# Kernel optimization log

Measured on AMD Instinct MI355X. Metric: run time of the kernel, lower is better.

Reference implementation:

```python
import jax, jax.numpy as jnp
import numpy as np

FRACTION = 0.33  # from attn_type='query_selector_0.33'


def setup_inputs() -> dict:
    key = jax.random.key(0)
    k1, k2, k3, k4 = jax.random.split(key, 4)
    B, L, DIM_VAL, DIM_ATTN = 8, 4096, 64, 64
    scale = 1.0 / np.sqrt(DIM_VAL).astype(np.float32)
    x = jax.random.normal(k1, (B, L, DIM_VAL), dtype=jnp.float32)
    Wq = jax.random.normal(k2, (DIM_VAL, DIM_ATTN), dtype=jnp.float32) * scale
    Wk = jax.random.normal(k3, (DIM_VAL, DIM_ATTN), dtype=jnp.float32) * scale
    Wv = jax.random.normal(k4, (DIM_VAL, DIM_VAL), dtype=jnp.float32) * scale
    return {"x": x, "Wq": Wq, "Wk": Wk, "Wv": Wv}


def reference(x, Wq, Wk, Wv):
    # Projections (bias-free Linears)
    Q = jnp.einsum('bld,de->ble', x, Wq)  # [B, L, Da]
    K = jnp.einsum('bld,de->ble', x, Wk)  # [B, L, Da]
    V = jnp.einsum('bld,de->ble', x, Wv)  # [B, L, Dv]

    B, L_Q, Da = Q.shape
    l_Q = int((1.0 - FRACTION) * L_Q)  # static: shapes known at trace time

    # keys.topk(l_Q, dim=1).values -> per-channel top-l_Q along seq; mean over them
    K_top = jax.lax.top_k(jnp.swapaxes(K, 1, 2), l_Q)[0]  # [B, Da, l_Q]
    K_reduce = K_top.mean(axis=-1)                         # [B, Da]

    # score each query against the reduced key; pick top-l_Q queries
    sqk = jnp.einsum('bd,bld->bl', K_reduce, Q)            # [B, L_Q]
    indices = jax.lax.top_k(sqk, l_Q)[1]                   # [B, l_Q] int32

    # gather sampled queries
    Q_sample = jnp.take_along_axis(Q, indices[:, :, None], axis=1)  # [B, l_Q, Da]

    # dense attention for the sampled queries only
    scores = jnp.einsum('bqd,bkd->bqk', Q_sample, K) / jnp.sqrt(jnp.asarray(Da, Q.dtype))
    attn = jax.nn.softmax(scores, axis=-1)                 # [B, l_Q, L]
    out_sel = jnp.einsum('bqk,bkv->bqv', attn, V)          # [B, l_Q, Dv]

    # mean-filled result, scatter attention outputs to selected rows
    mean_values = V.mean(axis=-2)                          # [B, Dv]
    result = jnp.broadcast_to(mean_values[:, None, :], (B, L_Q, V.shape[-1]))
    result = result.at[jnp.arange(B)[:, None], indices].set(out_sel)
    return result
```

## Files before the change

### kernel.cpp

```cpp
#include <hip/hip_runtime.h>
#include <hip/hip_bf16.h>
#include <math.h>

#define BATCH 8
#define SEQ   4096
#define DIM   64
#define LQ    2744
#define QPB   128
#define NQB   22
#define QPAD  2816
#define KS    8
#define L2E   1.4426950408889634f
#define QSC   0.1803368801111204f

typedef _Float16 half8 __attribute__((ext_vector_type(8)));
typedef short    bs8   __attribute__((ext_vector_type(8)));
typedef float    fx16  __attribute__((ext_vector_type(16)));
typedef unsigned short ushort_t;

union UH { uint4 u4; half8 h; };
union UB { unsigned u[4]; uint4 u4; bs8 s; };

__device__ __forceinline__ unsigned pack_bf16(float a, float b) {
    __hip_bfloat162 h = __float22bfloat162_rn(make_float2(a, b));
    union { __hip_bfloat162 h; unsigned u; } cv; cv.h = h; return cv.u;
}

__device__ __forceinline__ unsigned f2sort(float f) {
    unsigned u = __float_as_uint(f);
    return (u & 0x80000000u) ? ~u : (u | 0x80000000u);
}
__device__ __forceinline__ float sort2f(unsigned u) {
    return __uint_as_float((u & 0x80000000u) ? (u & 0x7FFFFFFFu) : ~u);
}

__device__ void radix_select_4096(const unsigned* u, int k, unsigned* hist,
                                  unsigned* wsum, unsigned* res, int pass_lo) {
    const int t = threadIdx.x;
    const int lane = t & 63, wv = t >> 6;
    if (t == 0) { res[0] = 0u; res[1] = (unsigned)k; }
    for (int pass = 3; pass >= pass_lo; --pass) {
        const int shift = pass * 8;
        hist[t] = 0u;
        __syncthreads();
        const unsigned pref  = res[0];
        const unsigned kk    = res[1];
        const unsigned hmask = (pass == 3) ? 0u : (0xFFFFFFFFu << (shift + 8));
        for (int i = t; i < 4096; i += 256) {
            unsigned ui = u[i];
            if ((ui & hmask) == pref) atomicAdd(&hist[(ui >> shift) & 255u], 1u);
        }
        __syncthreads();
        const unsigned h = hist[t];
        unsigned s = h;
#pragma unroll
        for (int ofs = 1; ofs < 64; ofs <<= 1) {
            unsigned a = __shfl_down(s, ofs, 64);
            s += (lane + ofs < 64) ? a : 0u;
        }
        if (lane == 0) wsum[wv] = s;
        __syncthreads();
#pragma unroll
        for (int w2 = 0; w2 < 4; ++w2)
            if (w2 > wv) s += wsum[w2];
        if (s >= kk && (s - h) < kk) {
            res[0] = pref | ((unsigned)t << shift);
            res[1] = kk - (s - h);
        }
        __syncthreads();
    }
}

__global__ __launch_bounds__(256) void proj_kernel(
    const float* __restrict__ x,  const float* __restrict__ Wq,
    const float* __restrict__ Wk, const float* __restrict__ Wv,
    float* __restrict__ Q, float* __restrict__ Kt,
    _Float16* __restrict__ Qh, _Float16* __restrict__ Kh,
    ushort_t* __restrict__ Vt, float* __restrict__ pmean) {
    const int rt = blockIdx.x, b = blockIdx.y, t = threadIdx.x;
    __shared__ float  red[4][64];
    const int ch = t & 63, rg = t >> 6;
    const float* xb = x + (size_t)b * SEQ * DIM;
    float accq[16], acck[16], accv[16];
#pragma unroll
    for (int i = 0; i < 16; ++i) { accq[i] = 0.f; acck[i] = 0.f; accv[i] = 0.f; }
    for (int dc = 0; dc < 4; ++dc) {
        float wq[16], wk[16], wv[16];
#pragma unroll
        for (int dd = 0; dd < 16; ++dd) {
            int d = dc * 16 + dd;
            wq[dd] = Wq[d * 64 + ch]; wk[dd] = Wk[d * 64 + ch]; wv[dd] = Wv[d * 64 + ch];
        }
        for (int r = 0; r < 16; ++r) {
            const int off = (rt * 64 + rg * 16 + r) * DIM + dc * 16;
            const float* xrow =
                xb + (unsigned)__builtin_amdgcn_readfirstlane(off);
            float xv[16];
#pragma unroll
            for (int dd = 0; dd < 16; ++dd) xv[dd] = xrow[dd];
#pragma unroll
            for (int dd = 0; dd < 16; ++dd) {
                accq[r] = fmaf(xv[dd], wq[dd], accq[r]);
                acck[r] = fmaf(xv[dd], wk[dd], acck[r]);
                accv[r] = fmaf(xv[dd], wv[dd], accv[r]);
            }
        }
    }
    const int rowbase = rt * 64 + rg * 16;
    float sv = 0.f;
#pragma unroll
    for (int r = 0; r < 16; ++r) {
        size_t o = ((size_t)b * SEQ + rowbase + r) * DIM + ch;
        Q[o]  = accq[r];
        Qh[o] = (_Float16)(accq[r] * QSC);
        Kh[o] = (_Float16)acck[r];
        sv += accv[r];
    }
    float4* ktp = (float4*)(Kt + ((size_t)b * 64 + ch) * SEQ + rowbase);
    ktp[0] = make_float4(acck[0], acck[1], acck[2], acck[3]);
    ktp[1] = make_float4(acck[4], acck[5], acck[6], acck[7]);
    ktp[2] = make_float4(acck[8], acck[9], acck[10], acck[11]);
    ktp[3] = make_float4(acck[12], acck[13], acck[14], acck[15]);
    {
        unsigned pk[8];
#pragma unroll
        for (int i = 0; i < 8; ++i) pk[i] = pack_bf16(accv[2*i], accv[2*i+1]);
        uint4* vp = (uint4*)(Vt + ((size_t)(b * 64 + ch)) * SEQ + rowbase);
        vp[0] = make_uint4(pk[0], pk[1], pk[4], pk[5]);
        vp[1] = make_uint4(pk[2], pk[3], pk[6], pk[7]);
    }
    red[rg][ch] = sv;
    __syncthreads();
    if (rg == 0)
        pmean[((size_t)b * 64 + ch) * 64 + rt] =
            red[0][ch] + red[1][ch] + red[2][ch] + red[3][ch];
}

__global__ __launch_bounds__(256) void kmean_kernel(const float* __restrict__ Kt,
                                                    const float* __restrict__ pmean,
                                                    float* __restrict__ Kred,
                                                    float* __restrict__ meanfin) {
    __shared__ unsigned u[4096];
    __shared__ unsigned hist[256];
    __shared__ unsigned wsum[4];
    __shared__ unsigned res[2];
    __shared__ float rsum[4];
    const int bc = blockIdx.x, t = threadIdx.x;
    if (t < 64) {
        float v = pmean[(size_t)bc * 64 + t];
        for (int m = 1; m < 64; m <<= 1) v += __shfl_xor(v, m, 64);
        if (t == 0) meanfin[bc] = v * (1.0f / (float)SEQ);
    }
    const float4* c4 = (const float4*)(Kt + (size_t)bc * SEQ);
    for (int i = t; i < 1024; i += 256) {
        float4 v = c4[i];
        u[i*4+0] = f2sort(v.x); u[i*4+1] = f2sort(v.y);
        u[i*4+2] = f2sort(v.z); u[i*4+3] = f2sort(v.w);
    }
    __syncthreads();
    radix_select_4096(u, LQ, hist, wsum, res, 2);
    const unsigned Tu = res[0];
    const int krem = (int)res[1];
    float loc = 0.f;
    for (int i = t; i < 4096; i += 256)
        if ((u[i] & 0xFFFF0000u) > Tu) loc += sort2f(u[i]);
    for (int msk = 1; msk < 64; msk <<= 1) loc += __shfl_xor(loc, msk, 64);
    if ((t & 63) == 0) rsum[t >> 6] = loc;
    __syncthreads();
    if (t == 0) {
        float s = rsum[0] + rsum[1] + rsum[2] + rsum[3]
                + (float)krem * sort2f(Tu | 0x8000u);
        Kred[bc] = s / (float)LQ;
    }
}

__global__ __launch_bounds__(256) void sqk_kernel(const float* __restrict__ Q,
                                                  const float* __restrict__ Kred,
                                                  float* __restrict__ sqk,
                                                  float4* __restrict__ pz) {
    const int b = blockIdx.y, l = blockIdx.x * 256 + threadIdx.x;
    __shared__ float kr[64];
    if (threadIdx.x < 64) kr[threadIdx.x] = Kred[b * 64 + threadIdx.x];
    {
        const int tid = (blockIdx.y * 16 + blockIdx.x) * 256 + threadIdx.x;
        const float4 z = make_float4(0.f, 0.f, 0.f, 0.f);
        for (int i = tid; i < 366080; i += 32768) pz[i] = z;
    }
    __syncthreads();
    const float4* q = (const float4*)(Q + ((size_t)b * SEQ + l) * DIM);
    float s = 0.f;
#pragma unroll
    for (int i = 0; i < 16; ++i) {
        float4 v = q[i];
        s = fmaf(v.x, kr[i*4+0], s); s = fmaf(v.y, kr[i*4+1], s);
        s = fmaf(v.z, kr[i*4+2], s); s = fmaf(v.w, kr[i*4+3], s);
    }
    sqk[b * SEQ + l] = s;
}

__global__ __launch_bounds__(256) void select_kernel(const float* __restrict__ sqk,
                                                     int* __restrict__ sel,
                                                     int* __restrict__ inv) {
    __shared__ unsigned u[4096];
    __shared__ unsigned hist[256];
    __shared__ unsigned wsum[4];
    __shared__ unsigned res[2];
    __shared__ int eq_idx[256];
    __shared__ int cnts[2];
    const int b = blockIdx.x, t = threadIdx.x;
    const float* col = sqk + (size_t)b * SEQ;
    int* invb = inv + (size_t)b * SEQ;
    for (int i = t; i < 4096; i += 256) {
        u[i] = f2sort(col[i]);
        invb[i] = -1;
    }
    if (t < 2) cnts[t] = 0;
    __syncthreads();
    radix_select_4096(u, LQ, hist, wsum, res, 0);
    const unsigned Tu = res[0];
    const int krem = (int)res[1];
    int* selb = sel + b * QPAD;
    for (int i = t; i < 4096; i += 256) {
        unsigned ui = u[i];
        if (ui > Tu) {
            int p = atomicAdd(&cnts[0], 1);
            selb[p] = i;
            invb[i] = p;
        } else if (ui == Tu) {
            int p = atomicAdd(&cnts[1], 1);
            if (p < 256) eq_idx[p] = i;
        }
    }
    __syncthreads();
    if (t == 0) {
        int ng = cnts[0];
        int ne = cnts[1] < 256 ? cnts[1] : 256;
        for (int i = 1; i < ne; ++i) {
            int v = eq_idx[i], j = i - 1;
            while (j >= 0 && eq_idx[j] > v) { eq_idx[j+1] = eq_idx[j]; --j; }
            eq_idx[j+1] = v;
        }
        for (int j = 0; j < krem; ++j) {
            selb[ng + j] = eq_idx[j];
            invb[eq_idx[j]] = ng + j;
        }
    }
    __syncthreads();
    if (t < QPAD - LQ) selb[LQ + t] = selb[LQ - 1];
}

__global__ __launch_bounds__(256, 4) void attn_kernel(
    const ushort_t* __restrict__ Qh, const ushort_t* __restrict__ Kh,
    const ushort_t* __restrict__ Vt, const int* __restrict__ sel,
    float* __restrict__ pl, float* __restrict__ pout) {
    const int lin = blockIdx.x + NQB * (blockIdx.y + KS * blockIdx.z);
    const int ks  = lin & 7;
    const int j8  = lin >> 3;
    const int b   = j8 / NQB;
    const int qt  = j8 % NQB;
    const int t = threadIdx.x, w = t >> 6, lane = t & 63;
    const int col = lane & 31, h = lane >> 5;

    __shared__ ushort_t Ktile[2][64 * 64];
    __shared__ ushort_t Vtile[2][2 * 32 * 64];

    half8 qf[4];
    {
        const int q = qt * QPB + w * 32 + col;
        const int row = sel[b * QPAD + q];
        const uint4* qg = (const uint4*)(Qh + ((size_t)b * SEQ + row) * DIM);
#pragma unroll
        for (int m = 0; m < 4; ++m) { UH u; u.u4 = qg[2 * m + h]; qf[m] = u.h; }
    }

    int koff[4], voff[4];
#pragma unroll
    for (int m = 0; m < 4; ++m)
        koff[m] = col * 64 + 8 * ((2 * m + h) ^ (col & 7));
#pragma unroll
    for (int i = 0; i < 4; ++i)
        voff[i] = col * 64 + 8 * ((i * 2 + h) ^ (col & 7));

    fx16 O0, O1;
#pragma unroll
    for (int r = 0; r < 16; ++r) { O0[r] = 0.f; O1[r] = 0.f; }
    float l = 0.f;

    const int srow = t >> 3, sgr = t & 7;
    const int lg = sgr ^ (srow & 7);
    const int vD = lg >> 2, vc = (lg >> 1) & 1, vh = lg & 1;
    const size_t kgbase = ((size_t)b * SEQ + ks * 512 + srow) * DIM + 8 * lg;
    const size_t vgbase = ((size_t)(b * DIM + srow + 32 * vD)) * SEQ
                          + ks * 512 + vc * 16 + vh * 8;

    uint4 kreg0 = *(const uint4*)(Kh + kgbase);
    uint4 kreg1 = *(const uint4*)(Kh + kgbase + 32 * DIM);
    uint4 vreg0 = *(const uint4*)(Vt + vgbase);
    uint4 vreg1 = *(const uint4*)(Vt + vgbase + 32);

    for (int tile = 0; tile < 8; ++tile) {
        const int buf = tile & 1;
        *(uint4*)&Ktile[buf][srow * 64 + sgr * 8]          = kreg0;
        *(uint4*)&Ktile[buf][(srow + 32) * 64 + sgr * 8]   = kreg1;
        *(uint4*)&Vtile[buf][srow * 64 + sgr * 8]          = vreg0;
        *(uint4*)&Vtile[buf][2048 + srow * 64 + sgr * 8]   = vreg1;
        __syncthreads();
        if (tile < 7) {
            const size_t ko = kgbase + (size_t)(tile + 1) * 64 * DIM;
            const size_t vo = vgbase + (size_t)(tile + 1) * 64;
            kreg0 = *(const uint4*)(Kh + ko);
            kreg1 = *(const uint4*)(Kh + ko + 32 * DIM);
            vreg0 = *(const uint4*)(Vt + vo);
            vreg1 = *(const uint4*)(Vt + vo + 32);
        }
#pragma unroll
        for (int ss = 0; ss < 2; ++ss) {
            const int so = ss * 2048;
            fx16 S;
#pragma unroll
            for (int r = 0; r < 16; ++r) S[r] = 0.f;
            __builtin_amdgcn_s_setprio(1);
#pragma unroll
            for (int m = 0; m < 4; ++m) {
                UH kf;
                kf.u4 = *(const uint4*)&Ktile[buf][koff[m] + so];
                S = __builtin_amdgcn_mfma_f32_32x32x16_f16(kf.h, qf[m], S, 0, 0, 0);
            }
            __builtin_amdgcn_s_setprio(0);
            float p[16];
#pragma unroll
            for (int r = 0; r < 16; ++r) p[r] = exp2f(S[r]);
#pragma unroll
            for (int r = 0; r < 16; ++r) l += p[r];
            UB A0, A1;
#pragma unroll
            for (int v = 0; v < 4; ++v) {
                A0.u[v] = pack_bf16(p[2 * v],     p[2 * v + 1]);
                A1.u[v] = pack_bf16(p[8 + 2 * v], p[8 + 2 * v + 1]);
            }
            __builtin_amdgcn_s_setprio(1);
#pragma unroll
            for (int D = 0; D < 2; ++D) {
                fx16& O = D ? O1 : O0;
#pragma unroll
                for (int c = 0; c < 2; ++c) {
                    UB vf;
                    vf.u4 = *(const uint4*)&Vtile[buf][voff[D * 2 + c] + so];
                    O = __builtin_amdgcn_mfma_f32_32x32x16_bf16(
                            c ? A1.s : A0.s, vf.s, O, 0, 0, 0);
                }
            }
            __builtin_amdgcn_s_setprio(0);
        }
        __syncthreads();
    }

    l += __shfl_xor(l, 32);

    const int qg0 = qt * QPB + w * 32;
    const size_t base = (size_t)b * QPAD + qg0;
#pragma unroll
    for (int D = 0; D < 2; ++D) {
        const fx16& O = D ? O1 : O0;
#pragma unroll
        for (int r = 0; r < 16; ++r) {
            const int q = (r & 3) + 8 * (r >> 2) + 4 * h;
            atomicAdd(&pout[(base + q) * DIM + D * 32 + col], O[r]);
        }
    }
    if (h == 0) atomicAdd(&pl[base + col], l);
}

__global__ __launch_bounds__(256) void comb_kernel(
    const float* __restrict__ pl, const float* __restrict__ pout,
    const int* __restrict__ inv, const float* __restrict__ meanfin,
    float* __restrict__ out) {
    const int idx = blockIdx.x * 256 + threadIdx.x;
    const int b = idx >> 16;
    const int rc = idx & 65535;
    const int row = rc >> 4, c = rc & 15;
    const int p = inv[b * SEQ + row];
    float4 o;
    if (p >= 0) {
        const size_t s0 = (size_t)b * QPAD + p;
        const float invl = 1.0f / pl[s0];
        float4 a = ((const float4*)(pout + s0 * DIM))[c];
        o = make_float4(a.x * invl, a.y * invl, a.z * invl, a.w * invl);
    } else {
        o = make_float4(meanfin[b * 64 + c * 4 + 0], meanfin[b * 64 + c * 4 + 1],
                        meanfin[b * 64 + c * 4 + 2], meanfin[b * 64 + c * 4 + 3]);
    }
    ((float4*)out)[idx] = o;
}

extern "C" void kernel_launch(void* const* d_in, const int* in_sizes, int n_in,
                              void* d_out, int out_size, void* d_ws, size_t ws_size,
                              hipStream_t stream) {
    const float* x  = (const float*)d_in[0];
    const float* Wq = (const float*)d_in[1];
    const float* Wk = (const float*)d_in[2];
    const float* Wv = (const float*)d_in[3];
    float* out = (float*)d_out;
    char* wsb  = (char*)d_ws;

    float*    Q       = (float*)(wsb);
    _Float16* Qh      = (_Float16*)(wsb + 8388608);
    _Float16* Kh      = (_Float16*)(wsb + 12582912);
    ushort_t* Vt      = (ushort_t*)(wsb + 16777216);
    float*    pmean   = (float*)(wsb + 20971520);
    float*    meanfin = (float*)(wsb + 21102592);
    float*    Kred    = (float*)(wsb + 21104640);
    float*    sqk     = (float*)(wsb + 21106688);
    int*      sel     = (int*)(wsb + 21237760);
    int*      inv     = (int*)(wsb + 21327872);
    float*    Kt      = (float*)(wsb + 21458944);
    float*    pout    = (float*)(wsb + 21458944);
    float*    pl      = (float*)(wsb + 21458944 + 5767168);

    proj_kernel  <<<dim3(64, 8),          256, 0, stream>>>(x, Wq, Wk, Wv, Q, Kt,
                                                            Qh, Kh, Vt, pmean);
    kmean_kernel <<<512,                  256, 0, stream>>>(Kt, pmean, Kred, meanfin);
    sqk_kernel   <<<dim3(16, 8),          256, 0, stream>>>(Q, Kred, sqk,
                                                            (float4*)pout);
    select_kernel<<<8,                    256, 0, stream>>>(sqk, sel, inv);
    attn_kernel  <<<dim3(NQB, KS, BATCH), 256, 0, stream>>>((const ushort_t*)Qh,
                                                            (const ushort_t*)Kh,
                                                            Vt, sel, pl, pout);
    comb_kernel  <<<2048,                 256, 0, stream>>>(pl, pout, inv, meanfin, out);
}
```

Measured before the change: 187.8 us.

## Halve attention block to 64 queries, 32-key tiles, drop trailing barrier

The attention kernel now uses 128-thread blocks that each handle 64 selected queries instead of 128, and it streams 32-key tiles over 16 iterations instead of 64-key tiles over 8. Query padding, the zero-fill range and workspace offsets are resized to match. The second __syncthreads per iteration is removed; the double-buffered LDS ordering still keeps overwrites safe. The goal is more workgroups with smaller LDS footprints for better occupancy and load balance, and less barrier overhead, at the cost of each K/V tile being reloaded by twice as many blocks.

```diff
diff --git a/kernel.cpp b/kernel.cpp
--- a/kernel.cpp
+++ b/kernel.cpp
@@ -6,9 +6,9 @@
 #define SEQ   4096
 #define DIM   64
 #define LQ    2744
-#define QPB   128
-#define NQB   22
-#define QPAD  2816
+#define QPB   64
+#define NQB   43
+#define QPAD  2752
 #define KS    8
 #define L2E   1.4426950408889634f
 #define QSC   0.1803368801111204f
@@ -184,7 +184,7 @@
     {
         const int tid = (blockIdx.y * 16 + blockIdx.x) * 256 + threadIdx.x;
         const float4 z = make_float4(0.f, 0.f, 0.f, 0.f);
-        for (int i = tid; i < 366080; i += 32768) pz[i] = z;
+        for (int i = tid; i < 357760; i += 32768) pz[i] = z;
     }
     __syncthreads();
     const float4* q = (const float4*)(Q + ((size_t)b * SEQ + l) * DIM);
@@ -249,7 +249,7 @@
     if (t < QPAD - LQ) selb[LQ + t] = selb[LQ - 1];
 }
 
-__global__ __launch_bounds__(256, 4) void attn_kernel(
+__global__ __launch_bounds__(128, 4) void attn_kernel(
     const ushort_t* __restrict__ Qh, const ushort_t* __restrict__ Kh,
     const ushort_t* __restrict__ Vt, const int* __restrict__ sel,
     float* __restrict__ pl, float* __restrict__ pout) {
@@ -261,8 +261,8 @@
     const int t = threadIdx.x, w = t >> 6, lane = t & 63;
     const int col = lane & 31, h = lane >> 5;
 
-    __shared__ ushort_t Ktile[2][64 * 64];
-    __shared__ ushort_t Vtile[2][2 * 32 * 64];
+    __shared__ ushort_t Ktile[2][32 * 64];
+    __shared__ ushort_t Vtile[2][32 * 64];
 
     half8 qf[4];
     {
@@ -286,73 +286,69 @@
     for (int r = 0; r < 16; ++r) { O0[r] = 0.f; O1[r] = 0.f; }
     float l = 0.f;
 
-    const int srow = t >> 3, sgr = t & 7;
-    const int lg = sgr ^ (srow & 7);
+    const int sr = t >> 3, sgr = t & 7;
+    const int lg = sgr ^ (sr & 7);
     const int vD = lg >> 2, vc = (lg >> 1) & 1, vh = lg & 1;
-    const size_t kgbase = ((size_t)b * SEQ + ks * 512 + srow) * DIM + 8 * lg;
-    const size_t vgbase = ((size_t)(b * DIM + srow + 32 * vD)) * SEQ
-                          + ks * 512 + vc * 16 + vh * 8;
-
-    uint4 kreg0 = *(const uint4*)(Kh + kgbase);
-    uint4 kreg1 = *(const uint4*)(Kh + kgbase + 32 * DIM);
-    uint4 vreg0 = *(const uint4*)(Vt + vgbase);
-    uint4 vreg1 = *(const uint4*)(Vt + vgbase + 32);
-
-    for (int tile = 0; tile < 8; ++tile) {
+    const size_t kg0 = ((size_t)b * SEQ + ks * 512 + sr) * DIM + 8 * lg;
+    const size_t kg1 = kg0 + 16 * DIM;
+    const size_t vg0 = ((size_t)(b * DIM + sr + 32 * vD)) * SEQ
+                       + ks * 512 + vc * 16 + vh * 8;
+    const size_t vg1 = vg0 + 16 * SEQ;
+
+    uint4 kr0 = *(const uint4*)(Kh + kg0);
+    uint4 kr1 = *(const uint4*)(Kh + kg1);
+    uint4 vr0 = *(const uint4*)(Vt + vg0);
+    uint4 vr1 = *(const uint4*)(Vt + vg1);
+
+    for (int tile = 0; tile < 16; ++tile) {
         const int buf = tile & 1;
-        *(uint4*)&Ktile[buf][srow * 64 + sgr * 8]          = kreg0;
-        *(uint4*)&Ktile[buf][(srow + 32) * 64 + sgr * 8]   = kreg1;
-        *(uint4*)&Vtile[buf][srow * 64 + sgr * 8]          = vreg0;
-        *(uint4*)&Vtile[buf][2048 + srow * 64 + sgr * 8]   = vreg1;
+        *(uint4*)&Ktile[buf][sr * 64 + sgr * 8]        = kr0;
+        *(uint4*)&Ktile[buf][(sr + 16) * 64 + sgr * 8] = kr1;
+        *(uint4*)&Vtile[buf][sr * 64 + sgr * 8]        = vr0;
+        *(uint4*)&Vtile[buf][(sr + 16) * 64 + sgr * 8] = vr1;
         __syncthreads();
-        if (tile < 7) {
-            const size_t ko = kgbase + (size_t)(tile + 1) * 64 * DIM;
-            const size_t vo = vgbase + (size_t)(tile + 1) * 64;
-            kreg0 = *(const uint4*)(Kh + ko);
-            kreg1 = *(const uint4*)(Kh + ko + 32 * DIM);
-            vreg0 = *(const uint4*)(Vt + vo);
-            vreg1 = *(const uint4*)(Vt + vo + 32);
-        }
-#pragma unroll
-        for (int ss = 0; ss < 2; ++ss) {
-            const int so = ss * 2048;
-            fx16 S;
-#pragma unroll
-            for (int r = 0; r < 16; ++r) S[r] = 0.f;
-            __builtin_amdgcn_s_setprio(1);
-#pragma unroll
-            for (int m = 0; m < 4; ++m) {
-                UH kf;
-                kf.u4 = *(const uint4*)&Ktile[buf][koff[m] + so];
-                S = __builtin_amdgcn_mfma_f32_32x32x16_f16(kf.h, qf[m], S, 0, 0, 0);
+        if (tile < 15) {
+            const size_t o = (size_t)(tile + 1) * 32;
+            kr0 = *(const uint4*)(Kh + kg0 + o * DIM);
+            kr1 = *(const uint4*)(Kh + kg1 + o * DIM);
+            vr0 = *(const uint4*)(Vt + vg0 + o);
+            vr1 = *(const uint4*)(Vt + vg1 + o);
+        }
+        fx16 S;
+#pragma unroll
+        for (int r = 0; r < 16; ++r) S[r] = 0.f;
+        __builtin_amdgcn_s_setprio(1);
+#pragma unroll
+        for (int m = 0; m < 4; ++m) {
+            UH kf;
+            kf.u4 = *(const uint4*)&Ktile[buf][koff[m]];
+            S = __builtin_amdgcn_mfma_f32_32x32x16_f16(kf.h, qf[m], S, 0, 0, 0);
+        }
+        __builtin_amdgcn_s_setprio(0);
+        float p[16];
+#pragma unroll
+        for (int r = 0; r < 16; ++r) p[r] = exp2f(S[r]);
+#pragma unroll
+        for (int r = 0; r < 16; ++r) l += p[r];
+        UB A0, A1;
+#pragma unroll
+        for (int v = 0; v < 4; ++v) {
+            A0.u[v] = pack_bf16(p[2 * v],     p[2 * v + 1]);
+            A1.u[v] = pack_bf16(p[8 + 2 * v], p[8 + 2 * v + 1]);
+        }
+        __builtin_amdgcn_s_setprio(1);
+#pragma unroll
+        for (int D = 0; D < 2; ++D) {
+            fx16& O = D ? O1 : O0;
+#pragma unroll
+            for (int c = 0; c < 2; ++c) {
+                UB vf;
+                vf.u4 = *(const uint4*)&Vtile[buf][voff[D * 2 + c]];
+                O = __builtin_amdgcn_mfma_f32_32x32x16_bf16(c ? A1.s : A0.s, vf.s,
+                                                            O, 0, 0, 0);
             }
-            __builtin_amdgcn_s_setprio(0);
-            float p[16];
-#pragma unroll
-            for (int r = 0; r < 16; ++r) p[r] = exp2f(S[r]);
-#pragma unroll
-            for (int r = 0; r < 16; ++r) l += p[r];
-            UB A0, A1;
-#pragma unroll
-            for (int v = 0; v < 4; ++v) {
-                A0.u[v] = pack_bf16(p[2 * v],     p[2 * v + 1]);
-                A1.u[v] = pack_bf16(p[8 + 2 * v], p[8 + 2 * v + 1]);
-            }
-            __builtin_amdgcn_s_setprio(1);
-#pragma unroll
-            for (int D = 0; D < 2; ++D) {
-                fx16& O = D ? O1 : O0;
-#pragma unroll
-                for (int c = 0; c < 2; ++c) {
-                    UB vf;
-                    vf.u4 = *(const uint4*)&Vtile[buf][voff[D * 2 + c] + so];
-                    O = __builtin_amdgcn_mfma_f32_32x32x16_bf16(
-                            c ? A1.s : A0.s, vf.s, O, 0, 0, 0);
-                }
-            }
-            __builtin_amdgcn_s_setprio(0);
-        }
-        __syncthreads();
+        }
+        __builtin_amdgcn_s_setprio(0);
     }
 
     l += __shfl_xor(l, 32);
@@ -415,7 +411,7 @@
     int*      inv     = (int*)(wsb + 21327872);
     float*    Kt      = (float*)(wsb + 21458944);
     float*    pout    = (float*)(wsb + 21458944);
-    float*    pl      = (float*)(wsb + 21458944 + 5767168);
+    float*    pl      = (float*)(wsb + 21458944 + 5636096);
 
     proj_kernel  <<<dim3(64, 8),          256, 0, stream>>>(x, Wq, Wk, Wv, Q, Kt,
                                                             Qh, Kh, Vt, pmean);
@@ -423,7 +419,7 @@
     sqk_kernel   <<<dim3(16, 8),          256, 0, stream>>>(Q, Kred, sqk,
                                                             (float4*)pout);
     select_kernel<<<8,                    256, 0, stream>>>(sqk, sel, inv);
-    attn_kernel  <<<dim3(NQB, KS, BATCH), 256, 0, stream>>>((const ushort_t*)Qh,
+    attn_kernel  <<<dim3(NQB, KS, BATCH), 128, 0, stream>>>((const ushort_t*)Qh,
                                                             (const ushort_t*)Kh,
                                                             Vt, sel, pl, pout);
     comb_kernel  <<<2048,                 256, 0, stream>>>(pl, pout, inv, meanfin, out);
```

New measurement: 192.0 us. +2.3%, slower.
